# Kernel optimization log

Hardware: AMD Instinct MI355X
Metric: run time of the kernel (lower is better)

Reference implementation:

```python
import jax, jax.numpy as jnp
import numpy as np

TOP_K = 2  # num_experts_per_tok


def setup_inputs() -> dict:
    key = jax.random.key(0)
    k1, k2, k3, k4, k5 = jax.random.split(key, 5)
    T, H, F, E = 2048, 2048, 1024, 8
    hidden_states = jax.random.normal(k1, (T, H), dtype=jnp.float32)
    router_logits = jax.random.normal(k2, (T, E), dtype=jnp.float32)
    s = 1.0 / np.sqrt(H)
    w1 = jax.random.normal(k3, (E, H, F), dtype=jnp.float32) * s  # gate proj
    w3 = jax.random.normal(k4, (E, H, F), dtype=jnp.float32) * s  # up proj
    w2 = jax.random.normal(k5, (E, F, H), dtype=jnp.float32) * (1.0 / np.sqrt(F))  # down proj
    return {"hidden_states": hidden_states, "router_logits": router_logits,
            "w1": w1, "w3": w3, "w2": w2}


def reference(hidden_states, router_logits, w1, w3, w2):
    # Top-K routing: softmax over raw logits, take top-k probs as combine weights
    # (renormalize_topk_logits=False, routed_scaling_factor=None).
    T, E = router_logits.shape
    probs = jax.nn.softmax(router_logits.astype(jnp.float32), axis=-1)  # (T, E)
    topk_w, topk_ids = jax.lax.top_k(probs, TOP_K)                      # (T, K)
    # Scatter combine weights into a dense (T, E) matrix (zeros off top-k).
    combine = jnp.zeros((T, E), dtype=probs.dtype).at[
        jnp.arange(T)[:, None], topk_ids].add(topk_w)                    # (T, E)

    x = hidden_states
    # SwiGLU expert FFN computed per-expert (dense over all tokens, masked by
    # combine weights -> same math as fused dispatch/grouped-GEMM/combine).
    g = jnp.einsum('th,ehf->etf', x, w1)          # (E, T, F) gate
    u = jnp.einsum('th,ehf->etf', x, w3)          # (E, T, F) up
    act = jax.nn.silu(g) * u                      # (E, T, F)
    act = act * combine.T[:, :, None]             # apply combine weight pre-down-proj
    y = jnp.einsum('etf,efh->th', act, w2)        # (T, H) combined over experts
    return y.astype(hidden_states.dtype)
```

## Files before the change

kernel.cpp:

```cpp
#include <hip/hip_runtime.h>
#include <stdint.h>

#define T_TOK 2048
#define HDIM  2048
#define FDIM  1024
#define NEXP  8

#define BM   64
#define BN   64
#define BK   32
#define NTHR 256
#define MT_MAX (T_TOK / BM)
#define NT1 (FDIM / BN)
#define NT2 (HDIM / BN)
#define NK1 (HDIM / BK)
#define NK2 (FDIM / BK)
#define GRID1 (NEXP * MT_MAX * NT1)
#define GRID2 (NEXP * MT_MAX * NT2)

typedef unsigned short u16;
typedef __attribute__((ext_vector_type(4))) float f32x4;
typedef __attribute__((ext_vector_type(8))) short bf16x8;
typedef __attribute__((ext_vector_type(8))) unsigned short u16x8;

__device__ __forceinline__ u16 f2bf(float f) {
  uint32_t u = __float_as_uint(f);
  u += 0x7FFFu + ((u >> 16) & 1u);
  return (u16)(u >> 16);
}

__device__ __forceinline__ void glds16(const u16* src, u16* dst) {
  __builtin_amdgcn_global_load_lds(
      (const __attribute__((address_space(1))) uint32_t*)src,
      (__attribute__((address_space(3))) uint32_t*)dst, 16, 0, 0);
}

__global__ void route1_kernel(const float* __restrict__ logits,
                              int* __restrict__ tok_e, float* __restrict__ tok_w,
                              int* __restrict__ counts) {
  __shared__ int lcnt[NEXP];
  const int tid = threadIdx.x;
  const int t = blockIdx.x * 256 + tid;
  if (tid < NEXP) lcnt[tid] = 0;
  __syncthreads();
  float l[NEXP];
#pragma unroll
  for (int e = 0; e < NEXP; ++e) l[e] = logits[t * NEXP + e];
  float m = l[0];
#pragma unroll
  for (int e = 1; e < NEXP; ++e) m = fmaxf(m, l[e]);
  float p[NEXP]; float s = 0.f;
#pragma unroll
  for (int e = 0; e < NEXP; ++e) { p[e] = __expf(l[e] - m); s += p[e]; }
  float inv = 1.f / s;
  int i0 = 0; float p0 = p[0];
#pragma unroll
  for (int e = 1; e < NEXP; ++e) if (p[e] > p0) { p0 = p[e]; i0 = e; }
  int i1 = -1; float p1 = -1.f;
#pragma unroll
  for (int e = 0; e < NEXP; ++e) if (e != i0 && p[e] > p1) { p1 = p[e]; i1 = e; }
  tok_e[t] = i0 | (i1 << 8);
  tok_w[t * 2]     = p0 * inv;
  tok_w[t * 2 + 1] = p1 * inv;
  atomicAdd(&lcnt[i0], 1);
  atomicAdd(&lcnt[i1], 1);
  __syncthreads();
  if (tid < NEXP) atomicAdd(&counts[tid], lcnt[tid]);
}

__global__ void route2_kernel(const int* __restrict__ counts,
                              int* __restrict__ offsets, int* __restrict__ cursor) {
  if (threadIdx.x == 0) {
    int s = 0;
    for (int e = 0; e < NEXP; ++e) { offsets[e] = s; cursor[e] = s; s += counts[e]; }
    offsets[NEXP] = s;
  }
}

__global__ void route3_kernel(const int* __restrict__ tok_e, const float* __restrict__ tok_w,
                              int* __restrict__ cursor,
                              int* __restrict__ token_list, float* __restrict__ slot_w) {
  __shared__ int lcnt[NEXP], lbase[NEXP];
  const int tid = threadIdx.x;
  const int t = blockIdx.x * 256 + tid;
  if (tid < NEXP) lcnt[tid] = 0;
  __syncthreads();
  int ee = tok_e[t];
  int e0 = ee & 255, e1 = ee >> 8;
  int li0 = atomicAdd(&lcnt[e0], 1);
  int li1 = atomicAdd(&lcnt[e1], 1);
  __syncthreads();
  if (tid < NEXP) lbase[tid] = atomicAdd(&cursor[tid], lcnt[tid]);
  __syncthreads();
  int s0 = lbase[e0] + li0;
  int s1 = lbase[e1] + li1;
  token_list[s0] = t; slot_w[s0] = tok_w[t * 2];
  token_list[s1] = t; slot_w[s1] = tok_w[t * 2 + 1];
}

__global__ void convert_x_kernel(const float4* __restrict__ x, ushort4* __restrict__ xb) {
  int i = blockIdx.x * 256 + threadIdx.x;
  float4 v = x[i];
  ushort4 o;
  o.x = f2bf(v.x); o.y = f2bf(v.y); o.z = f2bf(v.z); o.w = f2bf(v.w);
  xb[i] = o;
}

__global__ __launch_bounds__(NTHR, 4)
void gemm1_kernel(const u16* __restrict__ Xb,
                  const float* __restrict__ w1,
                  const float* __restrict__ w3,
                  const int* __restrict__ token_list,
                  const float* __restrict__ slot_w,
                  const int* __restrict__ counts,
                  const int* __restrict__ offsets,
                  u16* __restrict__ act) {
  const int bid = blockIdx.x;
  const int e  = bid >> 9;
  const int mt = (bid >> 4) & 31;
  const int nt = bid & 15;
  const int cnt = counts[e];
  if (mt * BM >= cnt) return;
  const int off = offsets[e];
  const int tid  = threadIdx.x;
  const int lane = tid & 63;
  const int wid  = tid >> 6;

  __shared__ u16 A_lds[2][BM * BK];
  __shared__ u16 B1_lds[BN * BK];
  __shared__ u16 B3_lds[BN * BK];

  const int rr = lane >> 2;
  {
  }
  const u16* a_src;
  {
    int mg = mt * BM + wid * 16 + rr;
    int mc = (mg < cnt) ? mg : (cnt - 1);
    int tok = token_list[off + mc];
    a_src = Xb + (size_t)tok * HDIM + (((lane & 3) ^ ((rr >> 1) & 3)) * 8);
  }

  const int colb = tid & 63;
  const int kq   = tid >> 6;
  const float* p1 = w1 + (size_t)e * HDIM * FDIM + (size_t)(kq * 8) * FDIM + nt * BN + colb;
  const float* p3 = w3 + (size_t)e * HDIM * FDIM + (size_t)(kq * 8) * FDIM + nt * BN + colb;
  u16* bw1 = &B1_lds[colb * BK + ((kq ^ ((colb >> 1) & 3)) * 8)];
  u16* bw3 = &B3_lds[colb * BK + ((kq ^ ((colb >> 1) & 3)) * 8)];

  const int wm = (wid >> 1) * 32;
  const int wn = (wid & 1) * 32;

  f32x4 accg[2][2] = {};
  f32x4 accu[2][2] = {};

  float v1[8], v3[8];
  glds16(a_src, &A_lds[0][wid * 512]);
#pragma unroll
  for (int i = 0; i < 8; ++i) v1[i] = p1[(size_t)i * FDIM];
#pragma unroll
  for (int i = 0; i < 8; ++i) v3[i] = p3[(size_t)i * FDIM];
  p1 += (size_t)BK * FDIM;
  p3 += (size_t)BK * FDIM;

#pragma unroll 1
  for (int t = 0; t < NK1; ++t) {
    u16x8 q;
#pragma unroll
    for (int i = 0; i < 8; ++i) q[i] = f2bf(v1[i]);
    *(u16x8*)bw1 = q;
#pragma unroll
    for (int i = 0; i < 8; ++i) q[i] = f2bf(v3[i]);
    *(u16x8*)bw3 = q;
    __syncthreads();

    if (t + 1 < NK1) {
      glds16(a_src + (t + 1) * BK, &A_lds[(t + 1) & 1][wid * 512]);
#pragma unroll
      for (int i = 0; i < 8; ++i) v1[i] = p1[(size_t)i * FDIM];
#pragma unroll
      for (int i = 0; i < 8; ++i) v3[i] = p3[(size_t)i * FDIM];
      p1 += (size_t)BK * FDIM;
      p3 += (size_t)BK * FDIM;
    }

    const u16* Ab = A_lds[t & 1];
    bf16x8 af[2], bg[2], bu[2];
#pragma unroll
    for (int m = 0; m < 2; ++m) {
      int R = wm + m * 16 + (lane & 15);
      af[m] = *(const bf16x8*)&Ab[R * BK + (((lane >> 4) ^ ((R >> 1) & 3)) * 8)];
    }
#pragma unroll
    for (int n = 0; n < 2; ++n) {
      int C = wn + n * 16 + (lane & 15);
      int pos = ((lane >> 4) ^ ((C >> 1) & 3)) * 8;
      bg[n] = *(const bf16x8*)&B1_lds[C * BK + pos];
      bu[n] = *(const bf16x8*)&B3_lds[C * BK + pos];
    }
#pragma unroll
    for (int m = 0; m < 2; ++m)
#pragma unroll
      for (int n = 0; n < 2; ++n) {
        accg[m][n] = __builtin_amdgcn_mfma_f32_16x16x32_bf16(af[m], bg[n], accg[m][n], 0, 0, 0);
        accu[m][n] = __builtin_amdgcn_mfma_f32_16x16x32_bf16(af[m], bu[n], accu[m][n], 0, 0, 0);
      }
    __syncthreads();
  }

  const int rb = mt * BM + wm;
#pragma unroll
  for (int m = 0; m < 2; ++m) {
#pragma unroll
    for (int j = 0; j < 4; ++j) {
      int mg = rb + m * 16 + (lane >> 4) * 4 + j;
      if (mg < cnt) {
        int slot = off + mg;
        float wgt = slot_w[slot];
#pragma unroll
        for (int n = 0; n < 2; ++n) {
          float g = accg[m][n][j];
          float u = accu[m][n][j];
          float sv = g / (1.f + __expf(-g));
          act[(size_t)slot * FDIM + nt * BN + wn + n * 16 + (lane & 15)] = f2bf(sv * u * wgt);
        }
      }
    }
  }
}

__global__ __launch_bounds__(NTHR, 4)
void gemm2_kernel(const u16* __restrict__ act,
                  const float* __restrict__ w2,
                  const int* __restrict__ token_list,
                  const int* __restrict__ counts,
                  const int* __restrict__ offsets,
                  float* __restrict__ y) {
  const int bid = blockIdx.x;
  const int e  = bid >> 10;
  const int mt = (bid >> 5) & 31;
  const int nt = bid & 31;
  const int cnt = counts[e];
  if (mt * BM >= cnt) return;
  const int off = offsets[e];
  const int tid  = threadIdx.x;
  const int lane = tid & 63;
  const int wid  = tid >> 6;

  __shared__ u16 A_lds[2][BM * BK];
  __shared__ u16 B_lds[BN * BK];

  const int rr = lane >> 2;
  const u16* a_src;
  {
    int mg = mt * BM + wid * 16 + rr;
    int mc = (mg < cnt) ? mg : (cnt - 1);
    a_src = act + (size_t)(off + mc) * FDIM + (((lane & 3) ^ ((rr >> 1) & 3)) * 8);
  }
  const int colb = tid & 63;
  const int kq   = tid >> 6;
  const float* p2 = w2 + (size_t)e * FDIM * HDIM + (size_t)(kq * 8) * HDIM + nt * BN + colb;
  u16* bw = &B_lds[colb * BK + ((kq ^ ((colb >> 1) & 3)) * 8)];

  const int wm = (wid >> 1) * 32;
  const int wn = (wid & 1) * 32;
  f32x4 acc[2][2] = {};

  float v[8];
  glds16(a_src, &A_lds[0][wid * 512]);
#pragma unroll
  for (int i = 0; i < 8; ++i) v[i] = p2[(size_t)i * HDIM];
  p2 += (size_t)BK * HDIM;

#pragma unroll 1
  for (int t = 0; t < NK2; ++t) {
    u16x8 q;
#pragma unroll
    for (int i = 0; i < 8; ++i) q[i] = f2bf(v[i]);
    *(u16x8*)bw = q;
    __syncthreads();

    if (t + 1 < NK2) {
      glds16(a_src + (t + 1) * BK, &A_lds[(t + 1) & 1][wid * 512]);
#pragma unroll
      for (int i = 0; i < 8; ++i) v[i] = p2[(size_t)i * HDIM];
      p2 += (size_t)BK * HDIM;
    }

    const u16* Ab = A_lds[t & 1];
    bf16x8 af[2], bb[2];
#pragma unroll
    for (int m = 0; m < 2; ++m) {
      int R = wm + m * 16 + (lane & 15);
      af[m] = *(const bf16x8*)&Ab[R * BK + (((lane >> 4) ^ ((R >> 1) & 3)) * 8)];
    }
#pragma unroll
    for (int n = 0; n < 2; ++n) {
      int C = wn + n * 16 + (lane & 15);
      bb[n] = *(const bf16x8*)&B_lds[C * BK + (((lane >> 4) ^ ((C >> 1) & 3)) * 8)];
    }
#pragma unroll
    for (int m = 0; m < 2; ++m)
#pragma unroll
      for (int n = 0; n < 2; ++n)
        acc[m][n] = __builtin_amdgcn_mfma_f32_16x16x32_bf16(af[m], bb[n], acc[m][n], 0, 0, 0);
    __syncthreads();
  }

  const int rb = mt * BM + wm;
#pragma unroll
  for (int m = 0; m < 2; ++m) {
#pragma unroll
    for (int j = 0; j < 4; ++j) {
      int mg = rb + m * 16 + (lane >> 4) * 4 + j;
      if (mg < cnt) {
        int slot = off + mg;
        int tok = token_list[slot];
        float* yp = y + (size_t)tok * HDIM + nt * BN + wn + (lane & 15);
#pragma unroll
        for (int n = 0; n < 2; ++n)
          unsafeAtomicAdd(yp + n * 16, acc[m][n][j]);
      }
    }
  }
}

extern "C" void kernel_launch(void* const* d_in, const int* in_sizes, int n_in,
                              void* d_out, int out_size, void* d_ws, size_t ws_size,
                              hipStream_t stream) {
  (void)in_sizes; (void)n_in; (void)out_size; (void)ws_size;
  const float* hs     = (const float*)d_in[0];
  const float* logits = (const float*)d_in[1];
  const float* w1     = (const float*)d_in[2];
  const float* w3     = (const float*)d_in[3];
  const float* w2     = (const float*)d_in[4];
  float* y = (float*)d_out;

  uint8_t* ws = (uint8_t*)d_ws;
  int*   token_list = (int*)(ws);
  float* slot_w     = (float*)(ws + (16 << 10));
  int*   counts     = (int*)(ws + (32 << 10));
  int*   offsets    = (int*)(ws + (32 << 10) + 128);
  int*   cursor     = (int*)(ws + (32 << 10) + 256);
  int*   tok_e      = (int*)(ws + (33 << 10));
  float* tok_w      = (float*)(ws + (42 << 10));
  u16*   Xb         = (u16*)(ws + (64 << 10));
  u16*   act        = (u16*)(ws + (64 << 10) + (size_t)T_TOK * HDIM * 2);

  hipMemsetAsync(counts, 0, NEXP * sizeof(int), stream);
  route1_kernel<<<T_TOK / 256, 256, 0, stream>>>(logits, tok_e, tok_w, counts);
  route2_kernel<<<1, 64, 0, stream>>>(counts, offsets, cursor);
  route3_kernel<<<T_TOK / 256, 256, 0, stream>>>(tok_e, tok_w, cursor, token_list, slot_w);
  convert_x_kernel<<<(T_TOK * HDIM / 4) / 256, 256, 0, stream>>>((const float4*)hs, (ushort4*)Xb);
  hipMemsetAsync(d_out, 0, (size_t)T_TOK * HDIM * sizeof(float), stream);
  gemm1_kernel<<<GRID1, NTHR, 0, stream>>>(Xb, w1, w3, token_list, slot_w, counts, offsets, act);
  gemm2_kernel<<<GRID2, NTHR, 0, stream>>>(act, w2, token_list, counts, offsets, y);
}
```

Measured before the change: 185.6 us.

## Pre-transpose weights to bf16 and use larger 32x32 MFMA tiles

Adds a transpose-and-convert kernel that turns w1, w3 and w2 into K-contiguous bf16 copies on every call. Both GEMMs can then stream A and B straight into LDS with global_load_lds, which removes the per-iteration fp32 loads and bf16 conversion inside the inner loop. The GEMM tiles grow to BM=128 and BK=64 and use the 32x32x16 bf16 MFMA with single-buffered LDS. The cost is an extra full pass over all expert weights each call, which reads the fp32 weights and writes bf16 copies, plus less overlap from the single LDS buffer.

```diff
diff --git a/kernel.cpp b/kernel.cpp
--- a/kernel.cpp
+++ b/kernel.cpp
@@ -6,11 +6,11 @@
 #define FDIM  1024
 #define NEXP  8
 
-#define BM   64
+#define BM   128
 #define BN   64
-#define BK   32
+#define BK   64
 #define NTHR 256
-#define MT_MAX (T_TOK / BM)
+#define MT_MAX 16
 #define NT1 (FDIM / BN)
 #define NT2 (HDIM / BN)
 #define NK1 (HDIM / BK)
@@ -19,9 +19,8 @@
 #define GRID2 (NEXP * MT_MAX * NT2)
 
 typedef unsigned short u16;
-typedef __attribute__((ext_vector_type(4))) float f32x4;
+typedef __attribute__((ext_vector_type(16))) float f32x16;
 typedef __attribute__((ext_vector_type(8))) short bf16x8;
-typedef __attribute__((ext_vector_type(8))) unsigned short u16x8;
 
 __device__ __forceinline__ u16 f2bf(float f) {
   uint32_t u = __float_as_uint(f);
@@ -106,18 +105,60 @@
   xb[i] = o;
 }
 
-__global__ __launch_bounds__(NTHR, 4)
+__global__ __launch_bounds__(256)
+void tconv_kernel(const float* __restrict__ src_, u16* __restrict__ dst_,
+                  int R, int C) {
+  const size_t msz = (size_t)R * C;
+  const float* src = src_ + blockIdx.z * msz;
+  u16* dst = dst_ + blockIdx.z * msz;
+  const int r0 = blockIdx.y * 64;
+  const int c0 = blockIdx.x * 64;
+  __shared__ uint32_t T[64][33];
+  const int t = threadIdx.x;
+  {
+    const int kp = t >> 3;
+    const int cg = t & 7;
+    const float* s0 = src + (size_t)(r0 + 2 * kp) * C + c0 + cg * 8;
+    float4 a0 = *(const float4*)(s0);
+    float4 a1 = *(const float4*)(s0 + 4);
+    float4 b0 = *(const float4*)(s0 + C);
+    float4 b1 = *(const float4*)(s0 + C + 4);
+    T[cg * 8 + 0][kp] = (uint32_t)f2bf(a0.x) | ((uint32_t)f2bf(b0.x) << 16);
+    T[cg * 8 + 1][kp] = (uint32_t)f2bf(a0.y) | ((uint32_t)f2bf(b0.y) << 16);
+    T[cg * 8 + 2][kp] = (uint32_t)f2bf(a0.z) | ((uint32_t)f2bf(b0.z) << 16);
+    T[cg * 8 + 3][kp] = (uint32_t)f2bf(a0.w) | ((uint32_t)f2bf(b0.w) << 16);
+    T[cg * 8 + 4][kp] = (uint32_t)f2bf(a1.x) | ((uint32_t)f2bf(b1.x) << 16);
+    T[cg * 8 + 5][kp] = (uint32_t)f2bf(a1.y) | ((uint32_t)f2bf(b1.y) << 16);
+    T[cg * 8 + 6][kp] = (uint32_t)f2bf(a1.z) | ((uint32_t)f2bf(b1.z) << 16);
+    T[cg * 8 + 7][kp] = (uint32_t)f2bf(a1.w) | ((uint32_t)f2bf(b1.w) << 16);
+  }
+  __syncthreads();
+  {
+    const int f = t >> 2;
+    const int kg = t & 3;
+    uint32_t v[8];
+#pragma unroll
+    for (int i = 0; i < 8; ++i) v[i] = T[f][kg * 8 + i];
+    u16* d = dst + (size_t)(c0 + f) * R + r0 + kg * 16;
+    uint4 w0 = {v[0], v[1], v[2], v[3]};
+    uint4 w1 = {v[4], v[5], v[6], v[7]};
+    *(uint4*)(d) = w0;
+    *(uint4*)(d + 8) = w1;
+  }
+}
+
+__global__ __launch_bounds__(NTHR, 3)
 void gemm1_kernel(const u16* __restrict__ Xb,
-                  const float* __restrict__ w1,
-                  const float* __restrict__ w3,
+                  const u16* __restrict__ w1t,
+                  const u16* __restrict__ w3t,
                   const int* __restrict__ token_list,
                   const float* __restrict__ slot_w,
                   const int* __restrict__ counts,
                   const int* __restrict__ offsets,
                   u16* __restrict__ act) {
   const int bid = blockIdx.x;
-  const int e  = bid >> 9;
-  const int mt = (bid >> 4) & 31;
+  const int e  = bid >> 8;
+  const int mt = (bid >> 4) & 15;
   const int nt = bid & 15;
   const int cnt = counts[e];
   if (mt * BM >= cnt) return;
@@ -125,105 +166,100 @@
   const int tid  = threadIdx.x;
   const int lane = tid & 63;
   const int wid  = tid >> 6;
-
-  __shared__ u16 A_lds[2][BM * BK];
+  const int wr = wid >> 1;
+  const int wc = wid & 1;
+
+  __shared__ u16 A_lds[BM * BK];
   __shared__ u16 B1_lds[BN * BK];
   __shared__ u16 B3_lds[BN * BK];
 
-  const int rr = lane >> 2;
-  {
-  }
-  const u16* a_src;
-  {
-    int mg = mt * BM + wid * 16 + rr;
+  const u16* a_src[4];
+#pragma unroll
+  for (int i = 0; i < 4; ++i) {
+    int row = (wid * 4 + i) * 8 + (lane >> 3);
+    int mg = mt * BM + row;
     int mc = (mg < cnt) ? mg : (cnt - 1);
     int tok = token_list[off + mc];
-    a_src = Xb + (size_t)tok * HDIM + (((lane & 3) ^ ((rr >> 1) & 3)) * 8);
-  }
-
-  const int colb = tid & 63;
-  const int kq   = tid >> 6;
-  const float* p1 = w1 + (size_t)e * HDIM * FDIM + (size_t)(kq * 8) * FDIM + nt * BN + colb;
-  const float* p3 = w3 + (size_t)e * HDIM * FDIM + (size_t)(kq * 8) * FDIM + nt * BN + colb;
-  u16* bw1 = &B1_lds[colb * BK + ((kq ^ ((colb >> 1) & 3)) * 8)];
-  u16* bw3 = &B3_lds[colb * BK + ((kq ^ ((colb >> 1) & 3)) * 8)];
-
-  const int wm = (wid >> 1) * 32;
-  const int wn = (wid & 1) * 32;
-
-  f32x4 accg[2][2] = {};
-  f32x4 accu[2][2] = {};
-
-  float v1[8], v3[8];
-  glds16(a_src, &A_lds[0][wid * 512]);
-#pragma unroll
-  for (int i = 0; i < 8; ++i) v1[i] = p1[(size_t)i * FDIM];
-#pragma unroll
-  for (int i = 0; i < 8; ++i) v3[i] = p3[(size_t)i * FDIM];
-  p1 += (size_t)BK * FDIM;
-  p3 += (size_t)BK * FDIM;
+    a_src[i] = Xb + (size_t)tok * HDIM + (((lane & 7) ^ (row & 7)) * 8);
+  }
+  const u16* b1_src[2];
+  const u16* b3_src[2];
+#pragma unroll
+  for (int i = 0; i < 2; ++i) {
+    int n = (wid * 2 + i) * 8 + (lane >> 3);
+    size_t rowoff = ((size_t)e * FDIM + nt * BN + n) * HDIM + (((lane & 7) ^ (n & 7)) * 8);
+    b1_src[i] = w1t + rowoff;
+    b3_src[i] = w3t + rowoff;
+  }
+
+  f32x16 accg[2] = {};
+  f32x16 accu[2] = {};
+
+#pragma unroll
+  for (int i = 0; i < 4; ++i) glds16(a_src[i], &A_lds[(wid * 4 + i) * 512]);
+#pragma unroll
+  for (int i = 0; i < 2; ++i) {
+    glds16(b1_src[i], &B1_lds[(wid * 2 + i) * 512]);
+    glds16(b3_src[i], &B3_lds[(wid * 2 + i) * 512]);
+  }
 
 #pragma unroll 1
   for (int t = 0; t < NK1; ++t) {
-    u16x8 q;
-#pragma unroll
-    for (int i = 0; i < 8; ++i) q[i] = f2bf(v1[i]);
-    *(u16x8*)bw1 = q;
-#pragma unroll
-    for (int i = 0; i < 8; ++i) q[i] = f2bf(v3[i]);
-    *(u16x8*)bw3 = q;
     __syncthreads();
-
+    bf16x8 af[2][4], bg[4], bu[4];
+#pragma unroll
+    for (int m = 0; m < 2; ++m) {
+      int R = wr * 64 + m * 32 + (lane & 31);
+#pragma unroll
+      for (int kk = 0; kk < 4; ++kk) {
+        int gl = kk * 2 + (lane >> 5);
+        af[m][kk] = *(const bf16x8*)&A_lds[R * BK + ((gl ^ (R & 7)) * 8)];
+      }
+    }
+    {
+      int R = wc * 32 + (lane & 31);
+#pragma unroll
+      for (int kk = 0; kk < 4; ++kk) {
+        int gl = kk * 2 + (lane >> 5);
+        int pos = R * BK + ((gl ^ (R & 7)) * 8);
+        bg[kk] = *(const bf16x8*)&B1_lds[pos];
+        bu[kk] = *(const bf16x8*)&B3_lds[pos];
+      }
+    }
+    __syncthreads();
     if (t + 1 < NK1) {
-      glds16(a_src + (t + 1) * BK, &A_lds[(t + 1) & 1][wid * 512]);
-#pragma unroll
-      for (int i = 0; i < 8; ++i) v1[i] = p1[(size_t)i * FDIM];
-#pragma unroll
-      for (int i = 0; i < 8; ++i) v3[i] = p3[(size_t)i * FDIM];
-      p1 += (size_t)BK * FDIM;
-      p3 += (size_t)BK * FDIM;
-    }
-
-    const u16* Ab = A_lds[t & 1];
-    bf16x8 af[2], bg[2], bu[2];
-#pragma unroll
-    for (int m = 0; m < 2; ++m) {
-      int R = wm + m * 16 + (lane & 15);
-      af[m] = *(const bf16x8*)&Ab[R * BK + (((lane >> 4) ^ ((R >> 1) & 3)) * 8)];
-    }
-#pragma unroll
-    for (int n = 0; n < 2; ++n) {
-      int C = wn + n * 16 + (lane & 15);
-      int pos = ((lane >> 4) ^ ((C >> 1) & 3)) * 8;
-      bg[n] = *(const bf16x8*)&B1_lds[C * BK + pos];
-      bu[n] = *(const bf16x8*)&B3_lds[C * BK + pos];
+      const int ks = (t + 1) * BK;
+#pragma unroll
+      for (int i = 0; i < 4; ++i) glds16(a_src[i] + ks, &A_lds[(wid * 4 + i) * 512]);
+#pragma unroll
+      for (int i = 0; i < 2; ++i) {
+        glds16(b1_src[i] + ks, &B1_lds[(wid * 2 + i) * 512]);
+        glds16(b3_src[i] + ks, &B3_lds[(wid * 2 + i) * 512]);
+      }
     }
 #pragma unroll
     for (int m = 0; m < 2; ++m)
 #pragma unroll
-      for (int n = 0; n < 2; ++n) {
-        accg[m][n] = __builtin_amdgcn_mfma_f32_16x16x32_bf16(af[m], bg[n], accg[m][n], 0, 0, 0);
-        accu[m][n] = __builtin_amdgcn_mfma_f32_16x16x32_bf16(af[m], bu[n], accu[m][n], 0, 0, 0);
-      }
-    __syncthreads();
-  }
-
-  const int rb = mt * BM + wm;
+      for (int kk = 0; kk < 4; ++kk) {
+        accg[m] = __builtin_amdgcn_mfma_f32_32x32x16_bf16(af[m][kk], bg[kk], accg[m], 0, 0, 0);
+        accu[m] = __builtin_amdgcn_mfma_f32_32x32x16_bf16(af[m][kk], bu[kk], accu[m], 0, 0, 0);
+      }
+  }
+
+  const int fcol = nt * BN + wc * 32 + (lane & 31);
 #pragma unroll
   for (int m = 0; m < 2; ++m) {
-#pragma unroll
-    for (int j = 0; j < 4; ++j) {
-      int mg = rb + m * 16 + (lane >> 4) * 4 + j;
+    int base = mt * BM + wr * 64 + m * 32 + 4 * (lane >> 5);
+#pragma unroll
+    for (int reg = 0; reg < 16; ++reg) {
+      int mg = base + (reg & 3) + 8 * (reg >> 2);
       if (mg < cnt) {
         int slot = off + mg;
         float wgt = slot_w[slot];
-#pragma unroll
-        for (int n = 0; n < 2; ++n) {
-          float g = accg[m][n][j];
-          float u = accu[m][n][j];
-          float sv = g / (1.f + __expf(-g));
-          act[(size_t)slot * FDIM + nt * BN + wn + n * 16 + (lane & 15)] = f2bf(sv * u * wgt);
-        }
+        float g = accg[m][reg];
+        float u = accu[m][reg];
+        float sv = g / (1.f + __expf(-g));
+        act[(size_t)slot * FDIM + fcol] = f2bf(sv * u * wgt);
       }
     }
   }
@@ -231,14 +267,14 @@
 
 __global__ __launch_bounds__(NTHR, 4)
 void gemm2_kernel(const u16* __restrict__ act,
-                  const float* __restrict__ w2,
+                  const u16* __restrict__ w2t,
                   const int* __restrict__ token_list,
                   const int* __restrict__ counts,
                   const int* __restrict__ offsets,
                   float* __restrict__ y) {
   const int bid = blockIdx.x;
-  const int e  = bid >> 10;
-  const int mt = (bid >> 5) & 31;
+  const int e  = bid >> 9;
+  const int mt = (bid >> 5) & 15;
   const int nt = bid & 31;
   const int cnt = counts[e];
   if (mt * BM >= cnt) return;
@@ -246,80 +282,81 @@
   const int tid  = threadIdx.x;
   const int lane = tid & 63;
   const int wid  = tid >> 6;
-
-  __shared__ u16 A_lds[2][BM * BK];
+  const int wr = wid >> 1;
+  const int wc = wid & 1;
+
+  __shared__ u16 A_lds[BM * BK];
   __shared__ u16 B_lds[BN * BK];
 
-  const int rr = lane >> 2;
-  const u16* a_src;
-  {
-    int mg = mt * BM + wid * 16 + rr;
+  const u16* a_src[4];
+#pragma unroll
+  for (int i = 0; i < 4; ++i) {
+    int row = (wid * 4 + i) * 8 + (lane >> 3);
+    int mg = mt * BM + row;
     int mc = (mg < cnt) ? mg : (cnt - 1);
-    a_src = act + (size_t)(off + mc) * FDIM + (((lane & 3) ^ ((rr >> 1) & 3)) * 8);
-  }
-  const int colb = tid & 63;
-  const int kq   = tid >> 6;
-  const float* p2 = w2 + (size_t)e * FDIM * HDIM + (size_t)(kq * 8) * HDIM + nt * BN + colb;
-  u16* bw = &B_lds[colb * BK + ((kq ^ ((colb >> 1) & 3)) * 8)];
-
-  const int wm = (wid >> 1) * 32;
-  const int wn = (wid & 1) * 32;
-  f32x4 acc[2][2] = {};
-
-  float v[8];
-  glds16(a_src, &A_lds[0][wid * 512]);
-#pragma unroll
-  for (int i = 0; i < 8; ++i) v[i] = p2[(size_t)i * HDIM];
-  p2 += (size_t)BK * HDIM;
+    a_src[i] = act + (size_t)(off + mc) * FDIM + (((lane & 7) ^ (row & 7)) * 8);
+  }
+  const u16* b_src[2];
+#pragma unroll
+  for (int i = 0; i < 2; ++i) {
+    int n = (wid * 2 + i) * 8 + (lane >> 3);
+    b_src[i] = w2t + ((size_t)e * HDIM + nt * BN + n) * FDIM + (((lane & 7) ^ (n & 7)) * 8);
+  }
+
+  f32x16 acc[2] = {};
+
+#pragma unroll
+  for (int i = 0; i < 4; ++i) glds16(a_src[i], &A_lds[(wid * 4 + i) * 512]);
+#pragma unroll
+  for (int i = 0; i < 2; ++i) glds16(b_src[i], &B_lds[(wid * 2 + i) * 512]);
 
 #pragma unroll 1
   for (int t = 0; t < NK2; ++t) {
-    u16x8 q;
-#pragma unroll
-    for (int i = 0; i < 8; ++i) q[i] = f2bf(v[i]);
-    *(u16x8*)bw = q;
     __syncthreads();
-
+    bf16x8 af[2][4], bb[4];
+#pragma unroll
+    for (int m = 0; m < 2; ++m) {
+      int R = wr * 64 + m * 32 + (lane & 31);
+#pragma unroll
+      for (int kk = 0; kk < 4; ++kk) {
+        int gl = kk * 2 + (lane >> 5);
+        af[m][kk] = *(const bf16x8*)&A_lds[R * BK + ((gl ^ (R & 7)) * 8)];
+      }
+    }
+    {
+      int R = wc * 32 + (lane & 31);
+#pragma unroll
+      for (int kk = 0; kk < 4; ++kk) {
+        int gl = kk * 2 + (lane >> 5);
+        bb[kk] = *(const bf16x8*)&B_lds[R * BK + ((gl ^ (R & 7)) * 8)];
+      }
+    }
+    __syncthreads();
     if (t + 1 < NK2) {
-      glds16(a_src + (t + 1) * BK, &A_lds[(t + 1) & 1][wid * 512]);
-#pragma unroll
-      for (int i = 0; i < 8; ++i) v[i] = p2[(size_t)i * HDIM];
-      p2 += (size_t)BK * HDIM;
-    }
-
-    const u16* Ab = A_lds[t & 1];
-    bf16x8 af[2], bb[2];
-#pragma unroll
-    for (int m = 0; m < 2; ++m) {
-      int R = wm + m * 16 + (lane & 15);
-      af[m] = *(const bf16x8*)&Ab[R * BK + (((lane >> 4) ^ ((R >> 1) & 3)) * 8)];
-    }
-#pragma unroll
-    for (int n = 0; n < 2; ++n) {
-      int C = wn + n * 16 + (lane & 15);
-      bb[n] = *(const bf16x8*)&B_lds[C * BK + (((lane >> 4) ^ ((C >> 1) & 3)) * 8)];
+      const int ks = (t + 1) * BK;
+#pragma unroll
+      for (int i = 0; i < 4; ++i) glds16(a_src[i] + ks, &A_lds[(wid * 4 + i) * 512]);
+#pragma unroll
+      for (int i = 0; i < 2; ++i) glds16(b_src[i] + ks, &B_lds[(wid * 2 + i) * 512]);
     }
 #pragma unroll
     for (int m = 0; m < 2; ++m)
 #pragma unroll
-      for (int n = 0; n < 2; ++n)
-        acc[m][n] = __builtin_amdgcn_mfma_f32_16x16x32_bf16(af[m], bb[n], acc[m][n], 0, 0, 0);
-    __syncthreads();
-  }
-
-  const int rb = mt * BM + wm;
+      for (int kk = 0; kk < 4; ++kk)
+        acc[m] = __builtin_amdgcn_mfma_f32_32x32x16_bf16(af[m][kk], bb[kk], acc[m], 0, 0, 0);
+  }
+
+  const int hcol = nt * BN + wc * 32 + (lane & 31);
 #pragma unroll
   for (int m = 0; m < 2; ++m) {
-#pragma unroll
-    for (int j = 0; j < 4; ++j) {
-      int mg = rb + m * 16 + (lane >> 4) * 4 + j;
+    int base = mt * BM + wr * 64 + m * 32 + 4 * (lane >> 5);
+#pragma unroll
+    for (int reg = 0; reg < 16; ++reg) {
+      int mg = base + (reg & 3) + 8 * (reg >> 2);
       if (mg < cnt) {
         int slot = off + mg;
         int tok = token_list[slot];
-        float* yp = y + (size_t)tok * HDIM + nt * BN + wn + (lane & 15);
-#pragma unroll
-        for (int n = 0; n < 2; ++n)
-          unsafeAtomicAdd(yp + n * 16, acc[m][n][j]);
+        unsafeAtomicAdd(y + (size_t)tok * HDIM + hcol, acc[m][reg]);
       }
     }
   }
@@ -344,15 +381,22 @@
   int*   cursor     = (int*)(ws + (32 << 10) + 256);
   int*   tok_e      = (int*)(ws + (33 << 10));
   float* tok_w      = (float*)(ws + (42 << 10));
-  u16*   Xb         = (u16*)(ws + (64 << 10));
-  u16*   act        = (u16*)(ws + (64 << 10) + (size_t)T_TOK * HDIM * 2);
+  const size_t MB = 1 << 20;
+  u16*   Xb  = (u16*)(ws + (64 << 10));
+  u16*   act = (u16*)(ws + (64 << 10) + 8 * MB);
+  u16*   w1t = (u16*)(ws + (64 << 10) + 16 * MB);
+  u16*   w3t = (u16*)(ws + (64 << 10) + 48 * MB);
+  u16*   w2t = (u16*)(ws + (64 << 10) + 80 * MB);
 
   hipMemsetAsync(counts, 0, NEXP * sizeof(int), stream);
   route1_kernel<<<T_TOK / 256, 256, 0, stream>>>(logits, tok_e, tok_w, counts);
   route2_kernel<<<1, 64, 0, stream>>>(counts, offsets, cursor);
   route3_kernel<<<T_TOK / 256, 256, 0, stream>>>(tok_e, tok_w, cursor, token_list, slot_w);
   convert_x_kernel<<<(T_TOK * HDIM / 4) / 256, 256, 0, stream>>>((const float4*)hs, (ushort4*)Xb);
+  tconv_kernel<<<dim3(FDIM / 64, HDIM / 64, NEXP), 256, 0, stream>>>(w1, w1t, HDIM, FDIM);
+  tconv_kernel<<<dim3(FDIM / 64, HDIM / 64, NEXP), 256, 0, stream>>>(w3, w3t, HDIM, FDIM);
+  tconv_kernel<<<dim3(HDIM / 64, FDIM / 64, NEXP), 256, 0, stream>>>(w2, w2t, FDIM, HDIM);
   hipMemsetAsync(d_out, 0, (size_t)T_TOK * HDIM * sizeof(float), stream);
-  gemm1_kernel<<<GRID1, NTHR, 0, stream>>>(Xb, w1, w3, token_list, slot_w, counts, offsets, act);
-  gemm2_kernel<<<GRID2, NTHR, 0, stream>>>(act, w2, token_list, counts, offsets, y);
-}
+  gemm1_kernel<<<GRID1, NTHR, 0, stream>>>(Xb, w1t, w3t, token_list, slot_w, counts, offsets, act);
+  gemm2_kernel<<<GRID2, NTHR, 0, stream>>>(act, w2t, token_list, counts, offsets, y);
+}
```

Measured after the change: 196.5 us. 1.06x slower.
